# Kernel optimization log

Measured on AMD Instinct MI355X. Metric: run time of the kernel, lower is better.

## Reference

```python
import jax, jax.numpy as jnp
import numpy as np

B, S, D, R = 256, 512, 128, 2048
H = 0.5  # integration step


def setup_inputs() -> dict:
    key = jax.random.key(0)
    ks = jax.random.split(key, 14)
    u = lambda k, shape, lo, hi: jax.random.uniform(k, shape, jnp.float32, lo, hi)
    bd, br = 1.0 / np.sqrt(D), 1.0 / np.sqrt(R)
    return {
        "inputs": jax.random.normal(ks[0], (B, S, D), jnp.float32),
        # input oscillator params (size D)
        "omega_in": u(ks[1], (D,), 1.0, 3.0),
        "gamma_in": u(ks[2], (D,), 0.1, 0.5),
        "alpha_in": u(ks[3], (D,), 0.5, 1.5),
        # input projection Linear(D -> R), torch layout [out, in]
        "W_proj": u(ks[4], (R, D), -bd, bd),
        "b_proj": u(ks[5], (R,), -bd, bd),
        # fixed reservoir oscillator params (size R)
        "omega_res": u(ks[6], (R,), 1.0, 3.0),
        "gamma_res": u(ks[7], (R,), 0.1, 0.5),
        "alpha_res": u(ks[8], (R,), 0.5, 1.5),
        # output oscillator params (size R)
        "omega_out": u(ks[9], (R,), 1.0, 3.0),
        "gamma_out": u(ks[10], (R,), 0.1, 0.5),
        "alpha_out": u(ks[11], (R,), 0.5, 1.5),
        # readout Linear(R -> D)
        "W_read": u(ks[12], (D, R), -br, br),
        "b_read": u(ks[13], (D,), -br, br),
    }


def _osc_step(f, x, y, omega, gamma, alpha):
    # x' = x + h*y ; y' = y + h*(alpha*f - 2|gamma|*y - |omega|^2 * x), clamped to [-5,5]
    accel = alpha * f - 2.0 * jnp.abs(gamma) * y - jnp.abs(omega) ** 2 * x
    x_new = jnp.clip(x + H * y, -5.0, 5.0)
    y_new = jnp.clip(y + H * accel, -5.0, 5.0)
    return x_new, y_new


def reference(inputs, omega_in, gamma_in, alpha_in, W_proj, b_proj,
              omega_res, gamma_res, alpha_res, omega_out, gamma_out, alpha_out,
              W_read, b_read):
    inputs_t = jnp.transpose(inputs, (1, 0, 2))  # [S, B, D]

    def step(carry, inp_t):
        x_in, y_in, x_res, y_res, x_out, y_out = carry
        x_in, y_in = _osc_step(inp_t, x_in, y_in, omega_in, gamma_in, alpha_in)
        proj = x_in @ W_proj.T + b_proj                      # [B, R]
        x_res, y_res = _osc_step(proj, x_res, y_res, omega_res, gamma_res, alpha_res)
        x_out, y_out = _osc_step(x_res, x_out, y_out, omega_out, gamma_out, alpha_out)
        pred = x_out @ W_read.T + b_read                     # [B, D]
        mse_out = jnp.mean((x_out - x_res) ** 2)             # scalar per step
        return (x_in, y_in, x_res, y_res, x_out, y_out), (pred, x_in, mse_out)

    z_d = jnp.zeros((B, D), inputs.dtype)
    z_r = jnp.zeros((B, R), inputs.dtype)
    carry0 = (z_d, z_d, z_r, z_r, z_r, z_r)
    _, (preds_t, x_in_seq, mse_out_seq) = jax.lax.scan(step, carry0, inputs_t)

    preds = jnp.transpose(preds_t, (1, 0, 2))  # [B, S, D]
    # pc_loss_in = sum_{t<S-1} mean((x_in(t) - inputs(t+1))^2)
    pc_loss_in = jnp.sum(jnp.mean((x_in_seq[:-1] - inputs_t[1:]) ** 2, axis=(1, 2)))
    pc_loss_out = jnp.sum(mse_out_seq)
    return preds, pc_loss_in, pc_loss_out
```

## Files before the change

kernel.cpp:

```cpp
#include <hip/hip_runtime.h>
#include <hip/hip_bf16.h>

#define Bn 256
#define Sn 512
#define Dn 128
#define Rn 2048
#define TB 32
#define NBLK (Sn / TB)
#define LDX 136
#define LDPs 1028
#define LDI 132
#define RG 1024

using bf16_t = __hip_bfloat16;
typedef short bf16x8 __attribute__((ext_vector_type(8)));
typedef float f32x4 __attribute__((ext_vector_type(4)));
typedef float f32x2 __attribute__((ext_vector_type(2)));

__device__ __forceinline__ f32x2 clip2(f32x2 v) {
  v = __builtin_elementwise_max(v, (f32x2)(-5.f));
  v = __builtin_elementwise_min(v, (f32x2)(5.f));
  return v;
}

__device__ __forceinline__ unsigned bf16rne(float f) {
  const unsigned u = __float_as_uint(f);
  return (u + 0x7fffu + ((u >> 16) & 1u)) >> 16;
}
__device__ __forceinline__ unsigned pack_bf16(f32x2 v) {
  return (bf16rne(v.y) << 16) | (bf16rne(v.x) & 0xffffu);
}

__global__ __launch_bounds__(256) void k_prep(const float* __restrict__ Wp,
                                              const float* __restrict__ Wr,
                                              bf16_t* __restrict__ Wp_b,
                                              bf16_t* __restrict__ Wr_b,
                                              float* __restrict__ losses) {
  const int i = blockIdx.x * 256 + threadIdx.x;
  Wp_b[i] = __float2bfloat16(Wp[i]);
  Wr_b[i] = __float2bfloat16(Wr[i]);
  if (i == 0) { losses[0] = 0.f; losses[1] = 0.f; }
}

__global__ __launch_bounds__(256) void k_zero(float* __restrict__ preds,
                                              const float* __restrict__ br) {
  const int i = blockIdx.x * 256 + threadIdx.x;
  const f32x4 bv = *(const f32x4*)(br + (i & 31) * 4);
  *((f32x4*)preds + i) = bv;
}

__global__ __launch_bounds__(512, 4) void k_fused(
    const float* __restrict__ inp,
    const float* __restrict__ om_i, const float* __restrict__ ga_i,
    const float* __restrict__ al_i,
    const bf16_t* __restrict__ Wp, const float* __restrict__ bp,
    const float* __restrict__ omr, const float* __restrict__ gar,
    const float* __restrict__ alr,
    const float* __restrict__ omo, const float* __restrict__ gao,
    const float* __restrict__ alo,
    const bf16_t* __restrict__ Wr,
    float* __restrict__ preds, float* __restrict__ losses) {
  __shared__ bf16_t Xs[TB * LDX];
  __shared__ bf16_t PX[TB * LDPs];
  __shared__ float bpS[RG];
  __shared__ float smi[8], smo[8];

  const int tid = threadIdx.x;
  const int b = blockIdx.x >> 1, g = blockIdx.x & 1;
  const int rbase = g * RG;
  const int wv = tid >> 6, lane = tid & 63;
  const int lr = lane & 15, lq = lane >> 4;

  for (int i = tid; i < RG; i += 512) bpS[i] = bp[rbase + i];

  float xi = 0.f, yi = 0.f, pc_in = 0.f;
  float w2i = 0.f, g2i = 0.f, ai = 0.f;
  if (tid < Dn) {
    w2i = om_i[tid] * om_i[tid];
    g2i = 2.f * fabsf(ga_i[tid]);
    ai = al_i[tid];
  }
  const float* inpb = inp + (size_t)b * Sn * Dn;

  const int rl = tid * 2;
  f32x2 xr = (f32x2)0.f, yr = (f32x2)0.f, xo = (f32x2)0.f, yo = (f32x2)0.f;
  f32x2 w2r, g2r, arv, w2o, g2o, aov;
  {
    f32x2 t;
    t = *(const f32x2*)(omr + rbase + rl); w2r = t * t;
    t = *(const f32x2*)(gar + rbase + rl); g2r = __builtin_elementwise_abs(t) * 2.f;
    arv = *(const f32x2*)(alr + rbase + rl);
    t = *(const f32x2*)(omo + rbase + rl); w2o = t * t;
    t = *(const f32x2*)(gao + rbase + rl); g2o = __builtin_elementwise_abs(t) * 2.f;
    aov = *(const f32x2*)(alo + rbase + rl);
  }
  f32x2 pc_out2 = (f32x2)0.f;

  float* Is = (float*)PX;

  __syncthreads();

  for (int blk = 0; blk < NBLK; ++blk) {
    const int t0 = blk * TB;

    {
      const float* src = inpb + (size_t)t0 * Dn;
      for (int i = tid; i < (TB * Dn) / 4; i += 512) {
        const int row = i >> 5, c4 = (i & 31) * 4;
        f32x4 v = __builtin_nontemporal_load((const f32x4*)(src + (size_t)row * Dn + c4));
        *(f32x4*)&Is[row * LDI + c4] = v;
      }
    }
    __syncthreads();

    if (tid < Dn) {
#pragma unroll
      for (int tt = 0; tt < TB; ++tt) {
        const float f = Is[tt * LDI + tid];
        if (t0 + tt > 0) { const float e = xi - f; pc_in += e * e; }
        const float accel = ai * f - g2i * yi - w2i * xi;
        const float xn = fminf(fmaxf(xi + 0.5f * yi, -5.f), 5.f);
        const float yn = fminf(fmaxf(yi + 0.5f * accel, -5.f), 5.f);
        Xs[tt * LDX + tid] = __float2bfloat16(xn);
        xi = xn; yi = yn;
      }
    }
    __syncthreads();

    {
      bf16x8 af[2][4];
#pragma unroll
      for (int i = 0; i < 2; ++i)
#pragma unroll
        for (int k = 0; k < 4; ++k)
          af[i][k] = *(const bf16x8*)&Xs[(i * 16 + lr) * LDX + k * 32 + lq * 8];

      const int lb = wv * 128;
      const bf16_t* wp_base = Wp + (size_t)(rbase + lb + lr) * Dn + lq * 8;
      bf16x8 bf[2][4];
#pragma unroll
      for (int k = 0; k < 4; ++k) {
        bf[0][k] = *(const bf16x8*)(wp_base + (size_t)0 * 16 * Dn + k * 32);
        bf[1][k] = *(const bf16x8*)(wp_base + (size_t)1 * 16 * Dn + k * 32);
      }
      for (int j = 0; j < 8; ++j) {
        const int pb = j & 1;
        f32x4 acc[2] = {(f32x4)0.f, (f32x4)0.f};
#pragma unroll
        for (int k = 0; k < 4; ++k) {
          acc[0] = __builtin_amdgcn_mfma_f32_16x16x32_bf16(af[0][k], bf[pb][k], acc[0], 0, 0, 0);
          acc[1] = __builtin_amdgcn_mfma_f32_16x16x32_bf16(af[1][k], bf[pb][k], acc[1], 0, 0, 0);
        }
        if (j + 2 < 8) {
#pragma unroll
          for (int k = 0; k < 4; ++k)
            bf[pb][k] = *(const bf16x8*)(wp_base + (size_t)(j + 2) * 16 * Dn + k * 32);
        }
        const int cl = lb + j * 16 + lr;
        const float bv = bpS[cl];
#pragma unroll
        for (int i = 0; i < 2; ++i)
#pragma unroll
          for (int r = 0; r < 4; ++r)
            PX[(i * 16 + lq * 4 + r) * LDPs + cl] = __float2bfloat16(acc[i][r] + bv);
      }
    }
    __syncthreads();

    {
      unsigned pk = *(unsigned*)&PX[0 * LDPs + rl];
      for (int tt = 0; tt < TB; ++tt) {
        unsigned pk_n = pk;
        if (tt + 1 < TB) pk_n = *(unsigned*)&PX[(tt + 1) * LDPs + rl];
        f32x2 pv;
        pv.x = __uint_as_float(pk << 16);
        pv.y = __uint_as_float(pk & 0xffff0000u);
        f32x2 acr = arv * pv - g2r * yr - w2r * xr;
        f32x2 xrn = clip2(xr + yr * 0.5f);
        f32x2 yrn = clip2(yr + acr * 0.5f);
        f32x2 aco = aov * xrn - g2o * yo - w2o * xo;
        f32x2 xon = clip2(xo + yo * 0.5f);
        f32x2 yon = clip2(yo + aco * 0.5f);
        f32x2 e = xon - xrn;
        pc_out2 += e * e;
        xr = xrn; yr = yrn; xo = xon; yo = yon;
        *(unsigned*)&PX[tt * LDPs + rl] = pack_bf16(xon);
        pk = pk_n;
      }
    }
    __syncthreads();

    {
      const int d0 = wv * 16;
      const bf16_t* wr_base = Wr + (size_t)(d0 + lr) * Rn + rbase + lq * 8;
      f32x4 acc[2][2] = {{(f32x4)0.f, (f32x4)0.f}, {(f32x4)0.f, (f32x4)0.f}};
      bf16x8 bcur = *(const bf16x8*)(wr_base);
#pragma unroll 2
      for (int k0 = 0; k0 < RG; k0 += 32) {
        bf16x8 bnxt = bcur;
        if (k0 + 32 < RG) bnxt = *(const bf16x8*)(wr_base + k0 + 32);
        const int par = (k0 >> 5) & 1;
        bf16x8 a0 = *(const bf16x8*)&PX[(0 + lr) * LDPs + k0 + lq * 8];
        bf16x8 a1 = *(const bf16x8*)&PX[(16 + lr) * LDPs + k0 + lq * 8];
        acc[0][par] = __builtin_amdgcn_mfma_f32_16x16x32_bf16(a0, bcur, acc[0][par], 0, 0, 0);
        acc[1][par] = __builtin_amdgcn_mfma_f32_16x16x32_bf16(a1, bcur, acc[1][par], 0, 0, 0);
        bcur = bnxt;
      }
      float* outb = preds + (size_t)b * Sn * Dn + (size_t)t0 * Dn;
      const int col = d0 + lr;
#pragma unroll
      for (int i = 0; i < 2; ++i) {
        f32x4 a = acc[i][0] + acc[i][1];
#pragma unroll
        for (int r = 0; r < 4; ++r) {
          const int row = i * 16 + lq * 4 + r;
          atomicAdd(outb + (size_t)row * Dn + col, a[r]);
        }
      }
    }
    __syncthreads();
  }

  float vi = pc_in;
  float vo = pc_out2.x + pc_out2.y;
#pragma unroll
  for (int o = 32; o > 0; o >>= 1) {
    vi += __shfl_down(vi, o, 64);
    vo += __shfl_down(vo, o, 64);
  }
  if (lane == 0) { smi[wv] = vi; smo[wv] = vo; }
  __syncthreads();
  if (tid == 0) {
    float si = 0.f, so = 0.f;
#pragma unroll
    for (int w = 0; w < 8; ++w) { si += smi[w]; so += smo[w]; }
    if (g == 0) atomicAdd(losses + 0, si * (1.f / ((float)Bn * (float)Dn)));
    atomicAdd(losses + 1, so * (1.f / ((float)Bn * (float)Rn)));
  }
}

extern "C" void kernel_launch(void* const* d_in, const int* in_sizes, int n_in,
                              void* d_out, int out_size, void* d_ws, size_t ws_size,
                              hipStream_t stream) {
  const float* inputs    = (const float*)d_in[0];
  const float* omega_in  = (const float*)d_in[1];
  const float* gamma_in  = (const float*)d_in[2];
  const float* alpha_in  = (const float*)d_in[3];
  const float* W_proj    = (const float*)d_in[4];
  const float* b_proj    = (const float*)d_in[5];
  const float* omega_res = (const float*)d_in[6];
  const float* gamma_res = (const float*)d_in[7];
  const float* alpha_res = (const float*)d_in[8];
  const float* omega_out = (const float*)d_in[9];
  const float* gamma_out = (const float*)d_in[10];
  const float* alpha_out = (const float*)d_in[11];
  const float* W_read    = (const float*)d_in[12];
  const float* b_read    = (const float*)d_in[13];

  float* out = (float*)d_out;
  float* losses = out + (size_t)Bn * Sn * Dn;

  bf16_t* Wp_b = (bf16_t*)d_ws;
  bf16_t* Wr_b = Wp_b + (size_t)Rn * Dn;

  k_prep<<<1024, 256, 0, stream>>>(W_proj, W_read, Wp_b, Wr_b, losses);
  k_zero<<<(Bn * Sn * Dn / 4) / 256, 256, 0, stream>>>(out, b_read);
  k_fused<<<Bn * 2, 512, 0, stream>>>(inputs, omega_in, gamma_in, alpha_in,
                                      Wp_b, b_proj,
                                      omega_res, gamma_res, alpha_res,
                                      omega_out, gamma_out, alpha_out,
                                      Wr_b, out, losses);
}
```

Before: 679.7 us.

## Split input oscillator into its own kernel and shard reservoir eight ways per batch

The input-oscillator recurrence moves into a separate kernel that writes bf16 x_in to workspace and accumulates the input loss. The fused kernel now splits the reservoir into 8 slices of 256 per batch row instead of 2 slices of 1024, giving 2048 blocks. It also doubles the time tile to 64 steps and prefetches the next x_in tile during the readout GEMM. The aim is more parallel blocks and no serial input-oscillator phase inside the fused loop. In exchange, the readout atomicAdds into preds rise fourfold, only two waves per block run the reservoir recurrence, and x_in makes an extra round trip through global memory.

```diff
diff --git a/kernel.cpp b/kernel.cpp
--- a/kernel.cpp
+++ b/kernel.cpp
@@ -5,12 +5,11 @@
 #define Sn 512
 #define Dn 128
 #define Rn 2048
-#define TB 32
-#define NBLK (Sn / TB)
-#define LDX 136
-#define LDPs 1028
-#define LDI 132
-#define RG 1024
+#define TBv 64
+#define NBLK (Sn / TBv)
+#define RG 256
+#define LDX 132
+#define LDPs 260
 
 using bf16_t = __hip_bfloat16;
 typedef short bf16x8 __attribute__((ext_vector_type(8)));
@@ -22,7 +21,6 @@
   v = __builtin_elementwise_min(v, (f32x2)(5.f));
   return v;
 }
-
 __device__ __forceinline__ unsigned bf16rne(float f) {
   const unsigned u = __float_as_uint(f);
   return (u + 0x7fffu + ((u >> 16) & 1u)) >> 16;
@@ -31,147 +29,155 @@
   return (bf16rne(v.y) << 16) | (bf16rne(v.x) & 0xffffu);
 }
 
-__global__ __launch_bounds__(256) void k_prep(const float* __restrict__ Wp,
+__global__ __launch_bounds__(256) void k_init(const float* __restrict__ Wp,
                                               const float* __restrict__ Wr,
+                                              const float* __restrict__ br,
                                               bf16_t* __restrict__ Wp_b,
                                               bf16_t* __restrict__ Wr_b,
+                                              float* __restrict__ preds,
                                               float* __restrict__ losses) {
-  const int i = blockIdx.x * 256 + threadIdx.x;
-  Wp_b[i] = __float2bfloat16(Wp[i]);
-  Wr_b[i] = __float2bfloat16(Wr[i]);
-  if (i == 0) { losses[0] = 0.f; losses[1] = 0.f; }
-}
-
-__global__ __launch_bounds__(256) void k_zero(float* __restrict__ preds,
-                                              const float* __restrict__ br) {
   const int i = blockIdx.x * 256 + threadIdx.x;
   const f32x4 bv = *(const f32x4*)(br + (i & 31) * 4);
   *((f32x4*)preds + i) = bv;
-}
-
-__global__ __launch_bounds__(512, 4) void k_fused(
-    const float* __restrict__ inp,
-    const float* __restrict__ om_i, const float* __restrict__ ga_i,
-    const float* __restrict__ al_i,
+  if (i < Rn * Dn) {
+    Wp_b[i] = __float2bfloat16(Wp[i]);
+    Wr_b[i] = __float2bfloat16(Wr[i]);
+  }
+  if (i == 0) { losses[0] = 0.f; losses[1] = 0.f; }
+}
+
+__global__ __launch_bounds__(128) void k_inosc(const float* __restrict__ inp,
+                                               const float* __restrict__ om,
+                                               const float* __restrict__ ga,
+                                               const float* __restrict__ al,
+                                               bf16_t* __restrict__ Xin,
+                                               float* __restrict__ loss_in) {
+  const int d = threadIdx.x, b = blockIdx.x;
+  const float w2 = om[d] * om[d];
+  const float g2 = 2.f * fabsf(ga[d]);
+  const float a = al[d];
+  const float* ip = inp + (size_t)b * Sn * Dn + d;
+  bf16_t* xp = Xin + (size_t)b * Sn * Dn + d;
+  float x = 0.f, y = 0.f, pc = 0.f;
+  float fv[16];
+#pragma unroll
+  for (int j = 0; j < 16; ++j) fv[j] = __builtin_nontemporal_load(ip + (size_t)j * Dn);
+  for (int tb = 0; tb < 32; ++tb) {
+    float fn[16];
+    if (tb < 31) {
+#pragma unroll
+      for (int j = 0; j < 16; ++j)
+        fn[j] = __builtin_nontemporal_load(ip + (size_t)((tb + 1) * 16 + j) * Dn);
+    }
+#pragma unroll
+    for (int j = 0; j < 16; ++j) {
+      const int t = tb * 16 + j;
+      const float f = fv[j];
+      if (t > 0) { const float e = x - f; pc += e * e; }
+      const float accel = a * f - g2 * y - w2 * x;
+      const float xn = fminf(fmaxf(x + 0.5f * y, -5.f), 5.f);
+      const float yn = fminf(fmaxf(y + 0.5f * accel, -5.f), 5.f);
+      xp[(size_t)t * Dn] = __float2bfloat16(xn);
+      x = xn; y = yn;
+    }
+#pragma unroll
+    for (int j = 0; j < 16; ++j) fv[j] = fn[j];
+  }
+#pragma unroll
+  for (int o = 32; o > 0; o >>= 1) pc += __shfl_down(pc, o, 64);
+  if ((threadIdx.x & 63) == 0)
+    atomicAdd(loss_in, pc * (1.f / ((float)Bn * (float)Dn)));
+}
+
+__global__ __launch_bounds__(512, 6) void k_fused(
+    const bf16_t* __restrict__ Xin,
     const bf16_t* __restrict__ Wp, const float* __restrict__ bp,
     const float* __restrict__ omr, const float* __restrict__ gar,
     const float* __restrict__ alr,
     const float* __restrict__ omo, const float* __restrict__ gao,
     const float* __restrict__ alo,
     const bf16_t* __restrict__ Wr,
-    float* __restrict__ preds, float* __restrict__ losses) {
-  __shared__ bf16_t Xs[TB * LDX];
-  __shared__ bf16_t PX[TB * LDPs];
+    float* __restrict__ preds, float* __restrict__ loss_out) {
+  __shared__ bf16_t Xs[TBv * LDX];
+  __shared__ bf16_t PX[TBv * LDPs];
   __shared__ float bpS[RG];
-  __shared__ float smi[8], smo[8];
+  __shared__ float smo[8];
 
   const int tid = threadIdx.x;
-  const int b = blockIdx.x >> 1, g = blockIdx.x & 1;
+  const int b = blockIdx.x >> 3, g = blockIdx.x & 7;
   const int rbase = g * RG;
   const int wv = tid >> 6, lane = tid & 63;
   const int lr = lane & 15, lq = lane >> 4;
 
-  for (int i = tid; i < RG; i += 512) bpS[i] = bp[rbase + i];
-
-  float xi = 0.f, yi = 0.f, pc_in = 0.f;
-  float w2i = 0.f, g2i = 0.f, ai = 0.f;
-  if (tid < Dn) {
-    w2i = om_i[tid] * om_i[tid];
-    g2i = 2.f * fabsf(ga_i[tid]);
-    ai = al_i[tid];
-  }
-  const float* inpb = inp + (size_t)b * Sn * Dn;
-
-  const int rl = tid * 2;
+  if (tid < RG) bpS[tid] = bp[rbase + tid];
+
   f32x2 xr = (f32x2)0.f, yr = (f32x2)0.f, xo = (f32x2)0.f, yo = (f32x2)0.f;
-  f32x2 w2r, g2r, arv, w2o, g2o, aov;
+  f32x2 w2r = (f32x2)0.f, g2r = (f32x2)0.f, arv = (f32x2)0.f;
+  f32x2 w2o = (f32x2)0.f, g2o = (f32x2)0.f, aov = (f32x2)0.f;
+  if (tid < 128) {
+    const int rg = rbase + tid * 2;
+    f32x2 t;
+    t = *(const f32x2*)(omr + rg); w2r = t * t;
+    t = *(const f32x2*)(gar + rg); g2r = __builtin_elementwise_abs(t) * 2.f;
+    arv = *(const f32x2*)(alr + rg);
+    t = *(const f32x2*)(omo + rg); w2o = t * t;
+    t = *(const f32x2*)(gao + rg); g2o = __builtin_elementwise_abs(t) * 2.f;
+    aov = *(const f32x2*)(alo + rg);
+  }
+  f32x2 pc_out2 = (f32x2)0.f;
+
+  const bf16_t* xinb = Xin + (size_t)b * Sn * Dn;
+
   {
-    f32x2 t;
-    t = *(const f32x2*)(omr + rbase + rl); w2r = t * t;
-    t = *(const f32x2*)(gar + rbase + rl); g2r = __builtin_elementwise_abs(t) * 2.f;
-    arv = *(const f32x2*)(alr + rbase + rl);
-    t = *(const f32x2*)(omo + rbase + rl); w2o = t * t;
-    t = *(const f32x2*)(gao + rbase + rl); g2o = __builtin_elementwise_abs(t) * 2.f;
-    aov = *(const f32x2*)(alo + rbase + rl);
-  }
-  f32x2 pc_out2 = (f32x2)0.f;
-
-  float* Is = (float*)PX;
-
+    const int c0 = tid, c1 = tid + 512;
+    *(uint4*)&Xs[(c0 >> 4) * LDX + (c0 & 15) * 8] =
+        *(const uint4*)(xinb + (size_t)(c0 >> 4) * Dn + (c0 & 15) * 8);
+    *(uint4*)&Xs[(c1 >> 4) * LDX + (c1 & 15) * 8] =
+        *(const uint4*)(xinb + (size_t)(c1 >> 4) * Dn + (c1 & 15) * 8);
+  }
   __syncthreads();
 
   for (int blk = 0; blk < NBLK; ++blk) {
-    const int t0 = blk * TB;
+    const int t0 = blk * TBv;
 
     {
-      const float* src = inpb + (size_t)t0 * Dn;
-      for (int i = tid; i < (TB * Dn) / 4; i += 512) {
-        const int row = i >> 5, c4 = (i & 31) * 4;
-        f32x4 v = __builtin_nontemporal_load((const f32x4*)(src + (size_t)row * Dn + c4));
-        *(f32x4*)&Is[row * LDI + c4] = v;
+      const int cb = wv * 32;
+#pragma unroll
+      for (int ct = 0; ct < 2; ++ct) {
+        const int cl = cb + ct * 16;
+        const bf16_t* wpb = Wp + (size_t)(rbase + cl + lr) * Dn + lq * 8;
+        bf16x8 bf[4];
+#pragma unroll
+        for (int k = 0; k < 4; ++k) bf[k] = *(const bf16x8*)(wpb + k * 32);
+        f32x4 acc[4];
+#pragma unroll
+        for (int rt = 0; rt < 4; ++rt) {
+          bf16x8 af[4];
+#pragma unroll
+          for (int k = 0; k < 4; ++k)
+            af[k] = *(const bf16x8*)&Xs[(rt * 16 + lr) * LDX + k * 32 + lq * 8];
+          f32x4 a = (f32x4)0.f;
+#pragma unroll
+          for (int k = 0; k < 4; ++k)
+            a = __builtin_amdgcn_mfma_f32_16x16x32_bf16(af[k], bf[k], a, 0, 0, 0);
+          acc[rt] = a;
+        }
+        const float bv = bpS[cl + lr];
+#pragma unroll
+        for (int rt = 0; rt < 4; ++rt)
+#pragma unroll
+          for (int r = 0; r < 4; ++r)
+            PX[(rt * 16 + lq * 4 + r) * LDPs + cl + lr] = __float2bfloat16(acc[rt][r] + bv);
       }
     }
     __syncthreads();
 
-    if (tid < Dn) {
-#pragma unroll
-      for (int tt = 0; tt < TB; ++tt) {
-        const float f = Is[tt * LDI + tid];
-        if (t0 + tt > 0) { const float e = xi - f; pc_in += e * e; }
-        const float accel = ai * f - g2i * yi - w2i * xi;
-        const float xn = fminf(fmaxf(xi + 0.5f * yi, -5.f), 5.f);
-        const float yn = fminf(fmaxf(yi + 0.5f * accel, -5.f), 5.f);
-        Xs[tt * LDX + tid] = __float2bfloat16(xn);
-        xi = xn; yi = yn;
-      }
-    }
-    __syncthreads();
-
-    {
-      bf16x8 af[2][4];
-#pragma unroll
-      for (int i = 0; i < 2; ++i)
-#pragma unroll
-        for (int k = 0; k < 4; ++k)
-          af[i][k] = *(const bf16x8*)&Xs[(i * 16 + lr) * LDX + k * 32 + lq * 8];
-
-      const int lb = wv * 128;
-      const bf16_t* wp_base = Wp + (size_t)(rbase + lb + lr) * Dn + lq * 8;
-      bf16x8 bf[2][4];
-#pragma unroll
-      for (int k = 0; k < 4; ++k) {
-        bf[0][k] = *(const bf16x8*)(wp_base + (size_t)0 * 16 * Dn + k * 32);
-        bf[1][k] = *(const bf16x8*)(wp_base + (size_t)1 * 16 * Dn + k * 32);
-      }
-      for (int j = 0; j < 8; ++j) {
-        const int pb = j & 1;
-        f32x4 acc[2] = {(f32x4)0.f, (f32x4)0.f};
-#pragma unroll
-        for (int k = 0; k < 4; ++k) {
-          acc[0] = __builtin_amdgcn_mfma_f32_16x16x32_bf16(af[0][k], bf[pb][k], acc[0], 0, 0, 0);
-          acc[1] = __builtin_amdgcn_mfma_f32_16x16x32_bf16(af[1][k], bf[pb][k], acc[1], 0, 0, 0);
-        }
-        if (j + 2 < 8) {
-#pragma unroll
-          for (int k = 0; k < 4; ++k)
-            bf[pb][k] = *(const bf16x8*)(wp_base + (size_t)(j + 2) * 16 * Dn + k * 32);
-        }
-        const int cl = lb + j * 16 + lr;
-        const float bv = bpS[cl];
-#pragma unroll
-        for (int i = 0; i < 2; ++i)
-#pragma unroll
-          for (int r = 0; r < 4; ++r)
-            PX[(i * 16 + lq * 4 + r) * LDPs + cl] = __float2bfloat16(acc[i][r] + bv);
-      }
-    }
-    __syncthreads();
-
-    {
+    if (tid < 128) {
+      const int rl = tid * 2;
       unsigned pk = *(unsigned*)&PX[0 * LDPs + rl];
-      for (int tt = 0; tt < TB; ++tt) {
+      for (int tt = 0; tt < TBv; ++tt) {
         unsigned pk_n = pk;
-        if (tt + 1 < TB) pk_n = *(unsigned*)&PX[(tt + 1) * LDPs + rl];
+        if (tt + 1 < TBv) pk_n = *(unsigned*)&PX[(tt + 1) * LDPs + rl];
         f32x2 pv;
         pv.x = __uint_as_float(pk << 16);
         pv.y = __uint_as_float(pk & 0xffff0000u);
@@ -190,52 +196,57 @@
     }
     __syncthreads();
 
+    uint4 sv0, sv1;
+    if (blk + 1 < NBLK) {
+      const bf16_t* src = xinb + (size_t)(t0 + TBv) * Dn;
+      const int c0 = tid, c1 = tid + 512;
+      sv0 = *(const uint4*)(src + (size_t)(c0 >> 4) * Dn + (c0 & 15) * 8);
+      sv1 = *(const uint4*)(src + (size_t)(c1 >> 4) * Dn + (c1 & 15) * 8);
+    }
+
     {
       const int d0 = wv * 16;
-      const bf16_t* wr_base = Wr + (size_t)(d0 + lr) * Rn + rbase + lq * 8;
-      f32x4 acc[2][2] = {{(f32x4)0.f, (f32x4)0.f}, {(f32x4)0.f, (f32x4)0.f}};
-      bf16x8 bcur = *(const bf16x8*)(wr_base);
-#pragma unroll 2
+      const bf16_t* wrb = Wr + (size_t)(d0 + lr) * Rn + rbase + lq * 8;
+      f32x4 acc[4] = {(f32x4)0.f, (f32x4)0.f, (f32x4)0.f, (f32x4)0.f};
+      bf16x8 bcur = *(const bf16x8*)(wrb);
+#pragma unroll
       for (int k0 = 0; k0 < RG; k0 += 32) {
         bf16x8 bnxt = bcur;
-        if (k0 + 32 < RG) bnxt = *(const bf16x8*)(wr_base + k0 + 32);
-        const int par = (k0 >> 5) & 1;
-        bf16x8 a0 = *(const bf16x8*)&PX[(0 + lr) * LDPs + k0 + lq * 8];
-        bf16x8 a1 = *(const bf16x8*)&PX[(16 + lr) * LDPs + k0 + lq * 8];
-        acc[0][par] = __builtin_amdgcn_mfma_f32_16x16x32_bf16(a0, bcur, acc[0][par], 0, 0, 0);
-        acc[1][par] = __builtin_amdgcn_mfma_f32_16x16x32_bf16(a1, bcur, acc[1][par], 0, 0, 0);
+        if (k0 + 32 < RG) bnxt = *(const bf16x8*)(wrb + k0 + 32);
+#pragma unroll
+        for (int rt = 0; rt < 4; ++rt) {
+          bf16x8 a = *(const bf16x8*)&PX[(rt * 16 + lr) * LDPs + k0 + lq * 8];
+          acc[rt] = __builtin_amdgcn_mfma_f32_16x16x32_bf16(a, bcur, acc[rt], 0, 0, 0);
+        }
         bcur = bnxt;
       }
       float* outb = preds + (size_t)b * Sn * Dn + (size_t)t0 * Dn;
       const int col = d0 + lr;
 #pragma unroll
-      for (int i = 0; i < 2; ++i) {
-        f32x4 a = acc[i][0] + acc[i][1];
-#pragma unroll
-        for (int r = 0; r < 4; ++r) {
-          const int row = i * 16 + lq * 4 + r;
-          atomicAdd(outb + (size_t)row * Dn + col, a[r]);
-        }
-      }
+      for (int rt = 0; rt < 4; ++rt)
+#pragma unroll
+        for (int r = 0; r < 4; ++r)
+          atomicAdd(outb + (size_t)(rt * 16 + lq * 4 + r) * Dn + col, acc[rt][r]);
+    }
+
+    if (blk + 1 < NBLK) {
+      const int c0 = tid, c1 = tid + 512;
+      *(uint4*)&Xs[(c0 >> 4) * LDX + (c0 & 15) * 8] = sv0;
+      *(uint4*)&Xs[(c1 >> 4) * LDX + (c1 & 15) * 8] = sv1;
     }
     __syncthreads();
   }
 
-  float vi = pc_in;
   float vo = pc_out2.x + pc_out2.y;
 #pragma unroll
-  for (int o = 32; o > 0; o >>= 1) {
-    vi += __shfl_down(vi, o, 64);
-    vo += __shfl_down(vo, o, 64);
-  }
-  if (lane == 0) { smi[wv] = vi; smo[wv] = vo; }
+  for (int o = 32; o > 0; o >>= 1) vo += __shfl_down(vo, o, 64);
+  if (lane == 0) smo[wv] = vo;
   __syncthreads();
   if (tid == 0) {
-    float si = 0.f, so = 0.f;
-#pragma unroll
-    for (int w = 0; w < 8; ++w) { si += smi[w]; so += smo[w]; }
-    if (g == 0) atomicAdd(losses + 0, si * (1.f / ((float)Bn * (float)Dn)));
-    atomicAdd(losses + 1, so * (1.f / ((float)Bn * (float)Rn)));
+    float so = 0.f;
+#pragma unroll
+    for (int w = 0; w < 8; ++w) so += smo[w];
+    atomicAdd(loss_out, so * (1.f / ((float)Bn * (float)Rn)));
   }
 }
 
@@ -262,12 +273,13 @@
 
   bf16_t* Wp_b = (bf16_t*)d_ws;
   bf16_t* Wr_b = Wp_b + (size_t)Rn * Dn;
-
-  k_prep<<<1024, 256, 0, stream>>>(W_proj, W_read, Wp_b, Wr_b, losses);
-  k_zero<<<(Bn * Sn * Dn / 4) / 256, 256, 0, stream>>>(out, b_read);
-  k_fused<<<Bn * 2, 512, 0, stream>>>(inputs, omega_in, gamma_in, alpha_in,
-                                      Wp_b, b_proj,
+  bf16_t* Xin  = Wr_b + (size_t)Rn * Dn;
+
+  k_init<<<(Bn * Sn * Dn / 4) / 256, 256, 0, stream>>>(W_proj, W_read, b_read,
+                                                       Wp_b, Wr_b, out, losses);
+  k_inosc<<<Bn, 128, 0, stream>>>(inputs, omega_in, gamma_in, alpha_in, Xin, losses);
+  k_fused<<<Bn * 8, 512, 0, stream>>>(Xin, Wp_b, b_proj,
                                       omega_res, gamma_res, alpha_res,
                                       omega_out, gamma_out, alpha_out,
-                                      Wr_b, out, losses);
-}
+                                      Wr_b, out, losses + 1);
+}
```

Measured after the change: 1.325 ms. +95.0%, slower.
